# Optimization experiments

Hardware: AMD Instinct MI355X
Metric: run time of the kernel (lower is better)

The kernel has to match this reference:

```python
import jax, jax.numpy as jnp
import numpy as np

B, J, E = 4096, 32, 256

def setup_inputs() -> dict:
    key = jax.random.key(0)
    ks = jax.random.split(key, 7)
    return {
        "x": jax.random.normal(ks[0], (B, E), dtype=jnp.float32),
        "state": jax.random.normal(ks[1], (B, J * E), dtype=jnp.float32),
        "keys": jax.random.normal(ks[2], (J, E), dtype=jnp.float32) * 0.1,
        "U": jax.random.normal(ks[3], (E, E), dtype=jnp.float32) * 0.1,
        "V": jax.random.normal(ks[4], (E, E), dtype=jnp.float32) * 0.1,
        "W": jax.random.normal(ks[5], (E, E), dtype=jnp.float32) * 0.1,
        "bias": jax.random.normal(ks[6], (E,), dtype=jnp.float32) * 0.1,
    }

def reference(x, state, keys, U, V, W, bias):
    b, je = state.shape
    j = keys.shape[0]
    e = x.shape[1]
    s = state.reshape(b, j, e)                      # [B,J,E]
    # gate_j = sigmoid(<x, state_j> + <x, key_j>)
    gate = jax.nn.sigmoid(jnp.einsum('be,bje->bj', x, s)
                          + x @ keys.T)             # [B,J]
    # candidate_j = relu(U s_j + bias + W x + V k_j)
    cand = jax.nn.relu(jnp.einsum('bje,fe->bjf', s, U)
                       + bias
                       + (x @ W.T)[:, None, :]
                       + (keys @ V.T)[None, :, :])  # [B,J,E]
    s_next = s + gate[..., None] * cand
    norm = jnp.abs(jnp.linalg.norm(s_next, axis=-1, keepdims=True)) + 1e-8
    s_next = s_next / norm
    return s_next.reshape(b, je)
```

## Files before the change

kernel.cpp:

```cpp
#include <hip/hip_runtime.h>
#include <hip/hip_bf16.h>

typedef __bf16 bf16_t;
typedef __attribute__((ext_vector_type(8))) __bf16 bf16x8;
typedef __attribute__((ext_vector_type(4))) float f32x4;

#define E_DIM 256
#define J_DIM 32
#define B_DIM 4096
#define M_DIM (B_DIM * J_DIM)
#define BM 64
#define BK 32
#define LDA 40
#define LDB 40
#define LDAF 33

__device__ inline bf16x8 cvt8(const float* __restrict__ p) {
    f32x4 a = *(const f32x4*)p;
    f32x4 b = *(const f32x4*)(p + 4);
    bf16x8 r;
    r[0] = (bf16_t)a[0]; r[1] = (bf16_t)a[1]; r[2] = (bf16_t)a[2]; r[3] = (bf16_t)a[3];
    r[4] = (bf16_t)b[0]; r[5] = (bf16_t)b[1]; r[6] = (bf16_t)b[2]; r[7] = (bf16_t)b[3];
    return r;
}

__global__ __launch_bounds__(256) void vkb_kernel(const float* __restrict__ keys,
                                                  const float* __restrict__ V,
                                                  const float* __restrict__ bias,
                                                  float* __restrict__ vkb) {
    int j = blockIdx.x, f = threadIdx.x;
    __shared__ float sk[E_DIM];
    sk[f] = keys[j * E_DIM + f];
    __syncthreads();
    float acc = bias[f];
    for (int e = 0; e < E_DIM; e += 4) {
        f32x4 vv = *(const f32x4*)(V + (size_t)f * E_DIM + e);
#pragma unroll
        for (int i = 0; i < 4; ++i) acc += vv[i] * sk[e + i];
    }
    vkb[(size_t)j * E_DIM + f] = acc;
}

__global__ __launch_bounds__(256) void xk_kernel(const float* __restrict__ x,
                                                 const float* __restrict__ keys,
                                                 float* __restrict__ xk) {
    __shared__ __align__(16) float sK[J_DIM][E_DIM];
    __shared__ __align__(16) float sX[8][E_DIM];
    int tid = threadIdx.x;
    int b0 = blockIdx.x * 8;
#pragma unroll
    for (int it = 0; it < 8; ++it) {
        int t = it * 256 + tid;
        *(f32x4*)(&sK[0][0] + (size_t)t * 4) = *(const f32x4*)(keys + (size_t)t * 4);
    }
#pragma unroll
    for (int it = 0; it < 2; ++it) {
        int t = it * 256 + tid;
        *(f32x4*)(&sX[0][0] + (size_t)t * 4) =
            *(const f32x4*)(x + (size_t)b0 * E_DIM + (size_t)t * 4);
    }
    __syncthreads();
    int j = tid & 31, bl = tid >> 5;
    float acc = 0.f;
    for (int e = 0; e < E_DIM; e += 4) {
        f32x4 xv = *(const f32x4*)(&sX[bl][e]);
        f32x4 kv = *(const f32x4*)(&sK[j][e]);
#pragma unroll
        for (int i = 0; i < 4; ++i) acc += xv[i] * kv[i];
    }
    xk[(size_t)(b0 + bl) * J_DIM + j] = acc;
}

__global__ __launch_bounds__(256) void wx_kernel(const float* __restrict__ x,
                                                 const float* __restrict__ W,
                                                 float* __restrict__ wx) {
    __shared__ __align__(16) bf16_t sA[BM][LDA];
    __shared__ __align__(16) bf16_t sB[E_DIM][LDB];
    int tid = threadIdx.x;
    int w = tid >> 6, lane = tid & 63, quad = lane >> 4, l15 = lane & 15;
    int m0 = blockIdx.x * BM;
    f32x4 acc[16];
#pragma unroll
    for (int nt = 0; nt < 16; ++nt)
#pragma unroll
        for (int r = 0; r < 4; ++r) acc[nt][r] = 0.f;
    int arow = tid >> 2, akk = (tid & 3) * 8;
    for (int kc = 0; kc < 8; ++kc) {
        int k0 = kc * BK;
        __syncthreads();
        *(bf16x8*)(&sA[arow][akk]) = cvt8(x + (size_t)(m0 + arow) * E_DIM + k0 + akk);
#pragma unroll
        for (int it = 0; it < 4; ++it) {
            int t = it * 256 + tid;
            int n = t >> 2, kk = (t & 3) * 8;
            *(bf16x8*)(&sB[n][kk]) = cvt8(W + (size_t)n * E_DIM + k0 + kk);
        }
        __syncthreads();
        bf16x8 af = *(const bf16x8*)(&sA[w * 16 + l15][quad * 8]);
#pragma unroll
        for (int nt = 0; nt < 16; ++nt) {
            bf16x8 bfr = *(const bf16x8*)(&sB[nt * 16 + l15][quad * 8]);
            acc[nt] = __builtin_amdgcn_mfma_f32_16x16x32_bf16(af, bfr, acc[nt], 0, 0, 0);
        }
    }
#pragma unroll
    for (int nt = 0; nt < 16; ++nt)
#pragma unroll
        for (int r = 0; r < 4; ++r)
            wx[(size_t)(m0 + w * 16 + quad * 4 + r) * E_DIM + nt * 16 + l15] = acc[nt][r];
}

__global__ __launch_bounds__(256) void memcell_kernel(
    const float* __restrict__ x, const float* __restrict__ state,
    const float* __restrict__ U, const float* __restrict__ wx,
    const float* __restrict__ xk, const float* __restrict__ vkb,
    float* __restrict__ out) {
    __shared__ __align__(16) bf16_t sA[BM][LDA];
    __shared__ __align__(16) bf16_t sB[E_DIM][LDB];
    __shared__ __align__(16) bf16_t sX[2][E_DIM];
    __shared__ __align__(16) float sAf[BM][LDAF];
    __shared__ __align__(16) float sXf[2][E_DIM];
    int tid = threadIdx.x;
    int w = tid >> 6, lane = tid & 63, quad = lane >> 4, l15 = lane & 15;
    int m0 = blockIdx.x * BM;
    int b0 = m0 >> 5;
    f32x4 acc[16];
#pragma unroll
    for (int nt = 0; nt < 16; ++nt)
#pragma unroll
        for (int r = 0; r < 4; ++r) acc[nt][r] = 0.f;
    float gdot = 0.f;
    if (tid < 64) {
        int bb = tid >> 5, p = tid & 31;
        f32x4 xa = *(const f32x4*)(x + (size_t)(b0 + bb) * E_DIM + p * 8);
        f32x4 xb = *(const f32x4*)(x + (size_t)(b0 + bb) * E_DIM + p * 8 + 4);
        *(f32x4*)(&sXf[bb][p * 8]) = xa;
        *(f32x4*)(&sXf[bb][p * 8 + 4]) = xb;
        bf16x8 r;
        r[0] = (bf16_t)xa[0]; r[1] = (bf16_t)xa[1]; r[2] = (bf16_t)xa[2]; r[3] = (bf16_t)xa[3];
        r[4] = (bf16_t)xb[0]; r[5] = (bf16_t)xb[1]; r[6] = (bf16_t)xb[2]; r[7] = (bf16_t)xb[3];
        *(bf16x8*)(&sX[bb][p * 8]) = r;
    }
    int arow = tid >> 2, akk = (tid & 3) * 8;
    for (int kc = 0; kc < 8; ++kc) {
        int k0 = kc * BK;
        __syncthreads();
        {
            const float* sp = state + (size_t)(m0 + arow) * E_DIM + k0 + akk;
            f32x4 a = *(const f32x4*)sp;
            f32x4 b = *(const f32x4*)(sp + 4);
            *(f32x4*)(&sAf[arow][akk]) = a;
            *(f32x4*)(&sAf[arow][akk + 4]) = b;
            bf16x8 r;
            r[0] = (bf16_t)a[0]; r[1] = (bf16_t)a[1]; r[2] = (bf16_t)a[2]; r[3] = (bf16_t)a[3];
            r[4] = (bf16_t)b[0]; r[5] = (bf16_t)b[1]; r[6] = (bf16_t)b[2]; r[7] = (bf16_t)b[3];
            *(bf16x8*)(&sA[arow][akk]) = r;
        }
#pragma unroll
        for (int it = 0; it < 4; ++it) {
            int t = it * 256 + tid;
            int n = t >> 2, kk = (t & 3) * 8;
            *(bf16x8*)(&sB[n][kk]) = cvt8(U + (size_t)n * E_DIM + k0 + kk);
        }
        __syncthreads();
        bf16x8 af = *(const bf16x8*)(&sA[w * 16 + l15][quad * 8]);
#pragma unroll
        for (int i = 0; i < 8; ++i)
            gdot += sAf[w * 16 + l15][quad * 8 + i] * sXf[w >> 1][k0 + quad * 8 + i];
#pragma unroll
        for (int nt = 0; nt < 16; ++nt) {
            bf16x8 bfr = *(const bf16x8*)(&sB[nt * 16 + l15][quad * 8]);
            acc[nt] = __builtin_amdgcn_mfma_f32_16x16x32_bf16(af, bfr, acc[nt], 0, 0, 0);
        }
    }
    gdot += __shfl_xor(gdot, 16);
    gdot += __shfl_xor(gdot, 32);
    int bw = b0 + (w >> 1);
    float garg = gdot + xk[(size_t)bw * J_DIM + (w & 1) * 16 + l15];
    float gv = 1.f / (1.f + expf(-garg));
    float gate[4];
#pragma unroll
    for (int r = 0; r < 4; ++r) gate[r] = __shfl(gv, quad * 4 + r);
    float sumsq[4] = {0.f, 0.f, 0.f, 0.f};
    const float* wxrow = wx + (size_t)bw * E_DIM;
#pragma unroll
    for (int nt = 0; nt < 16; ++nt) {
        int f = nt * 16 + l15;
        float wxf = wxrow[f];
#pragma unroll
        for (int r = 0; r < 4; ++r) {
            int rl = quad * 4 + r;
            int jidx = (w & 1) * 16 + rl;
            float c = acc[nt][r] + wxf + vkb[(size_t)jidx * E_DIM + f];
            c = fmaxf(c, 0.f);
            float sv = state[(size_t)(m0 + w * 16 + rl) * E_DIM + f];
            float t = fmaf(gate[r], c, sv);
            acc[nt][r] = t;
            sumsq[r] += t * t;
        }
    }
    float rn[4];
#pragma unroll
    for (int r = 0; r < 4; ++r) {
        float s2 = sumsq[r];
        s2 += __shfl_xor(s2, 1);
        s2 += __shfl_xor(s2, 2);
        s2 += __shfl_xor(s2, 4);
        s2 += __shfl_xor(s2, 8);
        rn[r] = 1.f / (sqrtf(s2) + 1e-8f);
    }
#pragma unroll
    for (int nt = 0; nt < 16; ++nt)
#pragma unroll
        for (int r = 0; r < 4; ++r)
            out[(size_t)(m0 + w * 16 + quad * 4 + r) * E_DIM + nt * 16 + l15] =
                acc[nt][r] * rn[r];
}

extern "C" void kernel_launch(void* const* d_in, const int* in_sizes, int n_in,
                              void* d_out, int out_size, void* d_ws, size_t ws_size,
                              hipStream_t stream) {
    const float* x     = (const float*)d_in[0];
    const float* state = (const float*)d_in[1];
    const float* keys  = (const float*)d_in[2];
    const float* U     = (const float*)d_in[3];
    const float* V     = (const float*)d_in[4];
    const float* W     = (const float*)d_in[5];
    const float* bias  = (const float*)d_in[6];
    float* out = (float*)d_out;

    float* wsf = (float*)d_ws;
    float* wx  = wsf;
    float* xk  = wsf + (size_t)B_DIM * E_DIM;
    float* vkb = xk + (size_t)B_DIM * J_DIM;

    vkb_kernel<<<J_DIM, 256, 0, stream>>>(keys, V, bias, vkb);
    xk_kernel<<<B_DIM / 8, 256, 0, stream>>>(x, keys, xk);
    wx_kernel<<<B_DIM / BM, 256, 0, stream>>>(x, W, wx);
    memcell_kernel<<<M_DIM / BM, 256, 0, stream>>>(x, state, U, wx, xk, vkb, out);
}
```

Measured before the change: 337.9 us.

## Merge prep kernels, pre-convert U to bf16, and load it via global_load_lds

Folds the three small precompute kernels (vkb, xk, wx) into one prep kernel, which also converts U to bf16 once in workspace. The main kernel now streams the bf16 U tile straight into shared memory with global_load_lds instead of having every block reload fp32 U and convert it. The gate dot product moves into registers during the state load, removing the fp32 shared-memory copy of the state tile. The aim is less global traffic, less conversion work, less LDS use and fewer launches. The risks are an unpadded sB layout that may cause LDS bank conflicts, and wx now being computed in scalar FP32 rather than with MFMA.

After: 373.6 us. 10.6% more time.

```diff
diff --git a/kernel.cpp b/kernel.cpp
--- a/kernel.cpp
+++ b/kernel.cpp
@@ -12,8 +12,6 @@
 #define BM 64
 #define BK 32
 #define LDA 40
-#define LDB 40
-#define LDAF 33
 
 __device__ inline bf16x8 cvt8(const float* __restrict__ p) {
     f32x4 a = *(const f32x4*)p;
@@ -24,101 +22,79 @@
     return r;
 }
 
-__global__ __launch_bounds__(256) void vkb_kernel(const float* __restrict__ keys,
-                                                  const float* __restrict__ V,
-                                                  const float* __restrict__ bias,
-                                                  float* __restrict__ vkb) {
-    int j = blockIdx.x, f = threadIdx.x;
-    __shared__ float sk[E_DIM];
-    sk[f] = keys[j * E_DIM + f];
-    __syncthreads();
-    float acc = bias[f];
-    for (int e = 0; e < E_DIM; e += 4) {
-        f32x4 vv = *(const f32x4*)(V + (size_t)f * E_DIM + e);
-#pragma unroll
-        for (int i = 0; i < 4; ++i) acc += vv[i] * sk[e + i];
-    }
-    vkb[(size_t)j * E_DIM + f] = acc;
-}
-
-__global__ __launch_bounds__(256) void xk_kernel(const float* __restrict__ x,
-                                                 const float* __restrict__ keys,
-                                                 float* __restrict__ xk) {
-    __shared__ __align__(16) float sK[J_DIM][E_DIM];
-    __shared__ __align__(16) float sX[8][E_DIM];
-    int tid = threadIdx.x;
-    int b0 = blockIdx.x * 8;
-#pragma unroll
-    for (int it = 0; it < 8; ++it) {
-        int t = it * 256 + tid;
-        *(f32x4*)(&sK[0][0] + (size_t)t * 4) = *(const f32x4*)(keys + (size_t)t * 4);
-    }
-#pragma unroll
-    for (int it = 0; it < 2; ++it) {
-        int t = it * 256 + tid;
-        *(f32x4*)(&sX[0][0] + (size_t)t * 4) =
-            *(const f32x4*)(x + (size_t)b0 * E_DIM + (size_t)t * 4);
-    }
-    __syncthreads();
-    int j = tid & 31, bl = tid >> 5;
-    float acc = 0.f;
-    for (int e = 0; e < E_DIM; e += 4) {
-        f32x4 xv = *(const f32x4*)(&sX[bl][e]);
-        f32x4 kv = *(const f32x4*)(&sK[j][e]);
-#pragma unroll
-        for (int i = 0; i < 4; ++i) acc += xv[i] * kv[i];
-    }
-    xk[(size_t)(b0 + bl) * J_DIM + j] = acc;
-}
-
-__global__ __launch_bounds__(256) void wx_kernel(const float* __restrict__ x,
-                                                 const float* __restrict__ W,
-                                                 float* __restrict__ wx) {
-    __shared__ __align__(16) bf16_t sA[BM][LDA];
-    __shared__ __align__(16) bf16_t sB[E_DIM][LDB];
-    int tid = threadIdx.x;
-    int w = tid >> 6, lane = tid & 63, quad = lane >> 4, l15 = lane & 15;
-    int m0 = blockIdx.x * BM;
-    f32x4 acc[16];
-#pragma unroll
-    for (int nt = 0; nt < 16; ++nt)
-#pragma unroll
-        for (int r = 0; r < 4; ++r) acc[nt][r] = 0.f;
-    int arow = tid >> 2, akk = (tid & 3) * 8;
-    for (int kc = 0; kc < 8; ++kc) {
-        int k0 = kc * BK;
-        __syncthreads();
-        *(bf16x8*)(&sA[arow][akk]) = cvt8(x + (size_t)(m0 + arow) * E_DIM + k0 + akk);
-#pragma unroll
-        for (int it = 0; it < 4; ++it) {
-            int t = it * 256 + tid;
-            int n = t >> 2, kk = (t & 3) * 8;
-            *(bf16x8*)(&sB[n][kk]) = cvt8(W + (size_t)n * E_DIM + k0 + kk);
-        }
-        __syncthreads();
-        bf16x8 af = *(const bf16x8*)(&sA[w * 16 + l15][quad * 8]);
-#pragma unroll
-        for (int nt = 0; nt < 16; ++nt) {
-            bf16x8 bfr = *(const bf16x8*)(&sB[nt * 16 + l15][quad * 8]);
-            acc[nt] = __builtin_amdgcn_mfma_f32_16x16x32_bf16(af, bfr, acc[nt], 0, 0, 0);
-        }
-    }
-#pragma unroll
-    for (int nt = 0; nt < 16; ++nt)
-#pragma unroll
-        for (int r = 0; r < 4; ++r)
-            wx[(size_t)(m0 + w * 16 + quad * 4 + r) * E_DIM + nt * 16 + l15] = acc[nt][r];
+__global__ __launch_bounds__(256) void prep_kernel(
+    const float* __restrict__ x, const float* __restrict__ keys,
+    const float* __restrict__ U, const float* __restrict__ V,
+    const float* __restrict__ W, const float* __restrict__ bias,
+    float* __restrict__ wx, float* __restrict__ xk,
+    float* __restrict__ vkb, bf16_t* __restrict__ Ub) {
+    int bid = blockIdx.x, tid = threadIdx.x;
+    if (bid < 256) {
+        __shared__ __align__(16) float sx[16][E_DIM + 4];
+        int b0 = bid * 16;
+        {
+            int r = tid >> 4, c = tid & 15;
+            const float* xp = x + (size_t)(b0 + r) * E_DIM + c * 16;
+#pragma unroll
+            for (int q = 0; q < 4; ++q)
+                *(f32x4*)(&sx[r][c * 16 + q * 4]) = *(const f32x4*)(xp + q * 4);
+        }
+        __syncthreads();
+        int f = tid;
+        float acc[16];
+#pragma unroll
+        for (int b = 0; b < 16; ++b) acc[b] = 0.f;
+        for (int e0 = 0; e0 < E_DIM; e0 += 8) {
+            f32x4 w0 = *(const f32x4*)(W + (size_t)f * E_DIM + e0);
+            f32x4 w1 = *(const f32x4*)(W + (size_t)f * E_DIM + e0 + 4);
+#pragma unroll
+            for (int b = 0; b < 16; ++b) {
+                float a = acc[b];
+#pragma unroll
+                for (int i = 0; i < 4; ++i) a = fmaf(w0[i], sx[b][e0 + i], a);
+#pragma unroll
+                for (int i = 0; i < 4; ++i) a = fmaf(w1[i], sx[b][e0 + 4 + i], a);
+                acc[b] = a;
+            }
+        }
+#pragma unroll
+        for (int b = 0; b < 16; ++b) wx[(size_t)(b0 + b) * E_DIM + f] = acc[b];
+        int j = tid & 31, bg = tid >> 5;
+        float a0 = 0.f, a1 = 0.f;
+        for (int e = 0; e < E_DIM; e += 4) {
+            f32x4 kv = *(const f32x4*)(keys + (size_t)j * E_DIM + e);
+            f32x4 x0 = *(const f32x4*)(&sx[bg * 2][e]);
+            f32x4 x1 = *(const f32x4*)(&sx[bg * 2 + 1][e]);
+#pragma unroll
+            for (int i = 0; i < 4; ++i) { a0 = fmaf(kv[i], x0[i], a0); a1 = fmaf(kv[i], x1[i], a1); }
+        }
+        xk[(size_t)(b0 + bg * 2) * J_DIM + j] = a0;
+        xk[(size_t)(b0 + bg * 2 + 1) * J_DIM + j] = a1;
+    } else if (bid < 288) {
+        int j = bid - 256, f = tid;
+        __shared__ float sk[E_DIM];
+        sk[f] = keys[(size_t)j * E_DIM + f];
+        __syncthreads();
+        float acc = bias[f];
+        for (int e = 0; e < E_DIM; e += 4) {
+            f32x4 vv = *(const f32x4*)(V + (size_t)f * E_DIM + e);
+#pragma unroll
+            for (int i = 0; i < 4; ++i) acc = fmaf(vv[i], sk[e + i], acc);
+        }
+        vkb[(size_t)j * E_DIM + f] = acc;
+    } else {
+        size_t idx = ((size_t)(bid - 288) * 256 + tid) * 8;
+        *(bf16x8*)(Ub + idx) = cvt8(U + idx);
+    }
 }
 
 __global__ __launch_bounds__(256) void memcell_kernel(
     const float* __restrict__ x, const float* __restrict__ state,
-    const float* __restrict__ U, const float* __restrict__ wx,
+    const bf16_t* __restrict__ Ub, const float* __restrict__ wx,
     const float* __restrict__ xk, const float* __restrict__ vkb,
     float* __restrict__ out) {
     __shared__ __align__(16) bf16_t sA[BM][LDA];
-    __shared__ __align__(16) bf16_t sB[E_DIM][LDB];
-    __shared__ __align__(16) bf16_t sX[2][E_DIM];
-    __shared__ __align__(16) float sAf[BM][LDAF];
+    __shared__ __align__(16) bf16_t sB[E_DIM][BK];
     __shared__ __align__(16) float sXf[2][E_DIM];
     int tid = threadIdx.x;
     int w = tid >> 6, lane = tid & 63, quad = lane >> 4, l15 = lane & 15;
@@ -129,59 +105,57 @@
     for (int nt = 0; nt < 16; ++nt)
 #pragma unroll
         for (int r = 0; r < 4; ++r) acc[nt][r] = 0.f;
-    float gdot = 0.f;
     if (tid < 64) {
         int bb = tid >> 5, p = tid & 31;
-        f32x4 xa = *(const f32x4*)(x + (size_t)(b0 + bb) * E_DIM + p * 8);
-        f32x4 xb = *(const f32x4*)(x + (size_t)(b0 + bb) * E_DIM + p * 8 + 4);
-        *(f32x4*)(&sXf[bb][p * 8]) = xa;
-        *(f32x4*)(&sXf[bb][p * 8 + 4]) = xb;
-        bf16x8 r;
-        r[0] = (bf16_t)xa[0]; r[1] = (bf16_t)xa[1]; r[2] = (bf16_t)xa[2]; r[3] = (bf16_t)xa[3];
-        r[4] = (bf16_t)xb[0]; r[5] = (bf16_t)xb[1]; r[6] = (bf16_t)xb[2]; r[7] = (bf16_t)xb[3];
-        *(bf16x8*)(&sX[bb][p * 8]) = r;
+        *(f32x4*)(&sXf[bb][p * 8]) = *(const f32x4*)(x + (size_t)(b0 + bb) * E_DIM + p * 8);
+        *(f32x4*)(&sXf[bb][p * 8 + 4]) = *(const f32x4*)(x + (size_t)(b0 + bb) * E_DIM + p * 8 + 4);
     }
     int arow = tid >> 2, akk = (tid & 3) * 8;
+    int bbs = arow >> 5;
+    float gpart = 0.f;
     for (int kc = 0; kc < 8; ++kc) {
         int k0 = kc * BK;
         __syncthreads();
+#pragma unroll
+        for (int is = 0; is < 4; ++is) {
+            int row = w * 64 + is * 16 + (lane >> 2);
+            const bf16_t* gp = Ub + (size_t)row * E_DIM + k0 + (lane & 3) * 8;
+            __builtin_amdgcn_global_load_lds(
+                (const __attribute__((address_space(1))) void*)gp,
+                (__attribute__((address_space(3))) void*)(&sB[w * 64 + is * 16][0]),
+                16, 0, 0);
+        }
         {
             const float* sp = state + (size_t)(m0 + arow) * E_DIM + k0 + akk;
             f32x4 a = *(const f32x4*)sp;
             f32x4 b = *(const f32x4*)(sp + 4);
-            *(f32x4*)(&sAf[arow][akk]) = a;
-            *(f32x4*)(&sAf[arow][akk + 4]) = b;
+#pragma unroll
+            for (int i = 0; i < 4; ++i) gpart = fmaf(a[i], sXf[bbs][k0 + akk + i], gpart);
+#pragma unroll
+            for (int i = 0; i < 4; ++i) gpart = fmaf(b[i], sXf[bbs][k0 + akk + 4 + i], gpart);
             bf16x8 r;
             r[0] = (bf16_t)a[0]; r[1] = (bf16_t)a[1]; r[2] = (bf16_t)a[2]; r[3] = (bf16_t)a[3];
             r[4] = (bf16_t)b[0]; r[5] = (bf16_t)b[1]; r[6] = (bf16_t)b[2]; r[7] = (bf16_t)b[3];
             *(bf16x8*)(&sA[arow][akk]) = r;
         }
-#pragma unroll
-        for (int it = 0; it < 4; ++it) {
-            int t = it * 256 + tid;
-            int n = t >> 2, kk = (t & 3) * 8;
-            *(bf16x8*)(&sB[n][kk]) = cvt8(U + (size_t)n * E_DIM + k0 + kk);
-        }
         __syncthreads();
         bf16x8 af = *(const bf16x8*)(&sA[w * 16 + l15][quad * 8]);
-#pragma unroll
-        for (int i = 0; i < 8; ++i)
-            gdot += sAf[w * 16 + l15][quad * 8 + i] * sXf[w >> 1][k0 + quad * 8 + i];
 #pragma unroll
         for (int nt = 0; nt < 16; ++nt) {
             bf16x8 bfr = *(const bf16x8*)(&sB[nt * 16 + l15][quad * 8]);
             acc[nt] = __builtin_amdgcn_mfma_f32_16x16x32_bf16(af, bfr, acc[nt], 0, 0, 0);
         }
     }
-    gdot += __shfl_xor(gdot, 16);
-    gdot += __shfl_xor(gdot, 32);
-    int bw = b0 + (w >> 1);
-    float garg = gdot + xk[(size_t)bw * J_DIM + (w & 1) * 16 + l15];
+    gpart += __shfl_xor(gpart, 1);
+    gpart += __shfl_xor(gpart, 2);
+    int grow = m0 + arow;
+    float garg = gpart + xk[(size_t)(grow >> 5) * J_DIM + (grow & 31)];
     float gv = 1.f / (1.f + expf(-garg));
     float gate[4];
 #pragma unroll
-    for (int r = 0; r < 4; ++r) gate[r] = __shfl(gv, quad * 4 + r);
+    for (int r = 0; r < 4; ++r) gate[r] = __shfl(gv, quad * 16 + r * 4);
     float sumsq[4] = {0.f, 0.f, 0.f, 0.f};
+    int bw = b0 + (w >> 1);
     const float* wxrow = wx + (size_t)bw * E_DIM;
 #pragma unroll
     for (int nt = 0; nt < 16; ++nt) {
@@ -230,12 +204,11 @@
     float* out = (float*)d_out;
 
     float* wsf = (float*)d_ws;
-    float* wx  = wsf;
-    float* xk  = wsf + (size_t)B_DIM * E_DIM;
-    float* vkb = xk + (size_t)B_DIM * J_DIM;
-
-    vkb_kernel<<<J_DIM, 256, 0, stream>>>(keys, V, bias, vkb);
-    xk_kernel<<<B_DIM / 8, 256, 0, stream>>>(x, keys, xk);
-    wx_kernel<<<B_DIM / BM, 256, 0, stream>>>(x, W, wx);
-    memcell_kernel<<<M_DIM / BM, 256, 0, stream>>>(x, state, U, wx, xk, vkb, out);
-}
+    float*  wx  = wsf;
+    float*  xk  = wsf + (size_t)B_DIM * E_DIM;
+    float*  vkb = xk + (size_t)B_DIM * J_DIM;
+    bf16_t* Ub  = (bf16_t*)(vkb + (size_t)J_DIM * E_DIM);
+
+    prep_kernel<<<320, 256, 0, stream>>>(x, keys, U, V, W, bias, wx, xk, vkb, Ub);
+    memcell_kernel<<<M_DIM / BM, 256, 0, stream>>>(x, state, Ub, wx, xk, vkb, out);
+}
```
